# Performance work log

Hardware: AMD Instinct MI355X
Metric: run time of the kernel (lower is better)

Reference implementation:

```python
import jax, jax.numpy as jnp
import numpy as np

B, LQ, E = 4, 8400, 256
HEADS, LEVELS, POINTS = 8, 4, 4
HEAD_DIM = E // HEADS
SHAPES = [(80, 80), (40, 40), (20, 20), (10, 10)]  # (H, W) per level; sum HW = 8400
LV = sum(h * w for h, w in SHAPES)


def setup_inputs() -> dict:
    key = jax.random.key(0)
    ks = jax.random.split(key, 12)
    query = jax.random.normal(ks[0], (B, LQ, E), jnp.float32)
    # per-level normalized reference points in (0.1, 0.9)
    reference_points = 0.1 + 0.8 * jax.random.uniform(ks[1], (B, LQ, LEVELS, 2), jnp.float32)
    value = jax.random.normal(ks[2], (B, LV, E), jnp.float32)
    spatial_shapes = jnp.array(SHAPES, dtype=jnp.int32)
    s = 0.05
    Wv = jax.random.normal(ks[3], (E, E), jnp.float32) * s
    bv = jnp.zeros((E,), jnp.float32)
    Woff = jax.random.normal(ks[4], (E, HEADS * LEVELS * POINTS * 2), jnp.float32) * 0.01
    boff = jax.random.normal(ks[5], (HEADS * LEVELS * POINTS * 2,), jnp.float32) * 0.02
    Wattn = jax.random.normal(ks[6], (E, HEADS * LEVELS * POINTS), jnp.float32) * s
    battn = jnp.zeros((HEADS * LEVELS * POINTS,), jnp.float32)
    Wo = jax.random.normal(ks[7], (E, E), jnp.float32) * s
    bo = jnp.zeros((E,), jnp.float32)
    return dict(query=query, reference_points=reference_points, value=value,
                spatial_shapes=spatial_shapes, Wv=Wv, bv=bv, Woff=Woff, boff=boff,
                Wattn=Wattn, battn=battn, Wo=Wo, bo=bo)


def _bilinear_sample(vflat, x, y, Hl, Wl):
    # vflat: [BH, D, Hl*Wl]; x, y: [BH, N] pixel coords (align_corners=False convention)
    x0f = jnp.floor(x); y0f = jnp.floor(y)
    wx = (x - x0f)[:, None, :]; wy = (y - y0f)[:, None, :]
    x0 = x0f.astype(jnp.int32); y0 = y0f.astype(jnp.int32)

    def gather(ix, iy):
        valid = ((ix >= 0) & (ix < Wl) & (iy >= 0) & (iy < Hl)).astype(vflat.dtype)
        idx = jnp.clip(iy, 0, Hl - 1) * Wl + jnp.clip(ix, 0, Wl - 1)
        g = jnp.take_along_axis(vflat, idx[:, None, :], axis=2)  # [BH, D, N]
        return g * valid[:, None, :]

    v00 = gather(x0, y0); v01 = gather(x0 + 1, y0)
    v10 = gather(x0, y0 + 1); v11 = gather(x0 + 1, y0 + 1)
    return (v00 * (1 - wx) * (1 - wy) + v01 * wx * (1 - wy)
            + v10 * (1 - wx) * wy + v11 * wx * wy)


def _msda_forward(query, reference_points, value, spatial_shapes,
                  Wv, bv, Woff, boff, Wattn, battn, Wo, bo):
    b, lq, _ = query.shape
    v = (value @ Wv + bv).reshape(b, -1, HEADS, HEAD_DIM)
    off = (query @ Woff + boff).reshape(b, lq, HEADS, LEVELS, POINTS, 2)
    aw = (query @ Wattn + battn).reshape(b, lq, HEADS, LEVELS * POINTS)
    aw = jax.nn.softmax(aw, axis=-1).reshape(b, lq, HEADS, LEVELS, POINTS)
    # normalizer (W, H) per level
    norm = jnp.stack([spatial_shapes[:, 1], spatial_shapes[:, 0]], axis=-1).astype(query.dtype)
    # sampling locations in [0,1]: [B, Lq, H, L, P, 2]
    loc = reference_points[:, :, None, :, None, :] + off / norm[None, None, None, :, None, :]

    sampled_levels = []
    start = 0
    for lvl, (Hl, Wl) in enumerate(SHAPES):
        vl = v[:, start:start + Hl * Wl]                      # [B, Hl*Wl, H, D]
        start += Hl * Wl
        vflat = vl.transpose(0, 2, 3, 1).reshape(b * HEADS, HEAD_DIM, Hl * Wl)
        grid = loc[:, :, :, lvl]                              # [B, Lq, H, P, 2]
        grid = grid.transpose(0, 2, 1, 3, 4).reshape(b * HEADS, lq * POINTS, 2)
        g = grid * 2.0 - 1.0                                  # grid_sample convention
        x = (g[..., 0] + 1.0) * (Wl * 0.5) - 0.5
        y = (g[..., 1] + 1.0) * (Hl * 0.5) - 0.5
        s = _bilinear_sample(vflat, x, y, Hl, Wl)             # [BH, D, Lq*P]
        sampled_levels.append(s.reshape(b, HEADS, HEAD_DIM, lq, POINTS))
    sampled = jnp.stack(sampled_levels, axis=-1)              # [B, H, D, Lq, P, L]
    out = jnp.einsum('bhdqpl,bqhlp->bqhd', sampled, aw).reshape(b, lq, E)
    return out @ Wo + bo


def reference(query, reference_points, value, spatial_shapes,
              Wv, bv, Woff, boff, Wattn, battn, Wo, bo):
    return _msda_forward(query, reference_points, value, spatial_shapes,
                         Wv, bv, Woff, boff, Wattn, battn, Wo, bo)
```

## Files before the change

kernel.cpp:

```cpp
#include <hip/hip_runtime.h>
#include <math.h>

#define BB 4
#define LQ 8400
#define NH 8
#define LVTOT 8500
#define HD 32

typedef __attribute__((ext_vector_type(8))) short short8;
typedef __attribute__((ext_vector_type(4))) float f32x4;
typedef __attribute__((ext_vector_type(2))) float f32x2;
typedef __attribute__((ext_vector_type(2))) _Float16 half2_t;
typedef __attribute__((ext_vector_type(2))) __fp16 fp16x2_t;
typedef unsigned short ushort_t;

__device__ __forceinline__ ushort_t f2bf(float f) {
    union { float f; unsigned u; } v; v.f = f;
    unsigned r = v.u + 0x7fffu + ((v.u >> 16) & 1u);
    return (ushort_t)(r >> 16);
}
__device__ __forceinline__ float bflo(unsigned u) {
    union { unsigned u; float f; } x; x.u = u << 16; return x.f;
}
__device__ __forceinline__ float bfhi(unsigned u) {
    union { unsigned u; float f; } x; x.u = u & 0xffff0000u; return x.f;
}
__device__ __forceinline__ half2_t ash2(unsigned u) {
    union { unsigned u; half2_t h; } x; x.u = u; return x.h;
}
__device__ __forceinline__ unsigned pk2u(fp16x2_t h) {
    union { fp16x2_t h; unsigned u; } x; x.h = h; return x.u;
}

__device__ __forceinline__ void dma16(const ushort_t* g, ushort_t* l) {
    __builtin_amdgcn_global_load_lds(
        (const __attribute__((address_space(1))) void*)g,
        (__attribute__((address_space(3))) void*)l, 16, 0, 0);
}

__global__ __launch_bounds__(256) void prep_all(
    const float* __restrict__ value, const float* __restrict__ query,
    const float* __restrict__ Wv, const float* __restrict__ Woff,
    const float* __restrict__ Wattn, const float* __restrict__ Wo,
    ushort_t* __restrict__ value_b, ushort_t* __restrict__ query_b,
    ushort_t* __restrict__ BT)
{
    const int bid = blockIdx.x;
    if (bid < 16900) {
        const float* src = (bid < 8500) ? value : query;
        ushort_t* dst = (bid < 8500) ? value_b : query_b;
        int i = (bid < 8500 ? bid : bid - 8500) * 256 + threadIdx.x;
        float4 f = ((const float4*)src)[i];
        ushort4 o;
        o.x = f2bf(f.x); o.y = f2bf(f.y); o.z = f2bf(f.z); o.w = f2bf(f.w);
        ((ushort4*)dst)[i] = o;
    } else {
        int idx = (bid - 16900) * 256 + threadIdx.x;
        int r = idx >> 8, k = idx & 255;
        float v;
        if (r < 256) v = Wv[k * 256 + r];
        else if (r < 640) {
            int n = r - 256;
            v = (n < 256) ? Woff[k * 256 + n] : Wattn[k * 128 + (n - 256)];
        } else v = Wo[k * 256 + (r - 640)];
        BT[idx] = f2bf(v);
    }
}

__device__ __forceinline__ void gemm_core(
    const ushort_t* __restrict__ A, const ushort_t* __restrict__ B, int M,
    int m0, int n0, ushort_t* Asl, ushort_t* Bsl, f32x4 acc[4][4])
{
    const int tid  = threadIdx.x;
    const int wave = tid >> 6, lane = tid & 63;
    const int quad = lane >> 4, mr = lane & 15;
    const int wm   = (wave >> 1) * 64, wn = (wave & 1) * 64;
    const int oct  = lane >> 3;
    const int bseg = lane & 7;

    for (int k0 = 0; k0 < 256; k0 += 64) {
        __syncthreads();
        #pragma unroll
        for (int i = 0; i < 4; i++) {
            int m  = i * 32 + wave * 8 + oct;
            int gs = bseg ^ (m & 7);
            int am = min(m0 + m, M - 1);
            dma16(A + (size_t)am * 256 + k0 + gs * 8,
                  Asl + (size_t)(i * 32 + wave * 8) * 64 + lane * 8);
            int bn = n0 + m;
            dma16(B + (size_t)bn * 256 + k0 + gs * 8,
                  Bsl + (size_t)(i * 32 + wave * 8) * 64 + lane * 8);
        }
        __syncthreads();
        #pragma unroll
        for (int ks = 0; ks < 2; ks++) {
            short8 af[4], bf[4];
            const int ksl = ks * 4 + quad;
            #pragma unroll
            for (int i = 0; i < 4; i++) {
                int m = wm + i * 16 + mr;
                af[i] = *(const short8*)&Asl[m * 64 + (ksl ^ (m & 7)) * 8];
                int n = wn + i * 16 + mr;
                bf[i] = *(const short8*)&Bsl[n * 64 + (ksl ^ (n & 7)) * 8];
            }
            #pragma unroll
            for (int i = 0; i < 4; i++)
                #pragma unroll
                for (int j = 0; j < 4; j++)
                    acc[i][j] = __builtin_amdgcn_mfma_f32_16x16x32_bf16(
                        af[i], bf[j], acc[i][j], 0, 0, 0);
        }
    }
}

__global__ __launch_bounds__(256, 3) void gemm_fused(
    const ushort_t* __restrict__ Av, const ushort_t* __restrict__ Aq,
    const ushort_t* __restrict__ BT,
    const float* __restrict__ bv, const float* __restrict__ boff,
    const float* __restrict__ battn,
    ushort_t* __restrict__ vperm, ushort_t* __restrict__ off_b,
    ushort_t* __restrict__ awl_b)
{
    __shared__ ushort_t Asl[128 * 64];
    __shared__ ushort_t Bsl[128 * 64];

    const int bid = blockIdx.x;
    int mode, m0, n0, M;
    const ushort_t *A, *B;
    if (bid < 532) { mode = 0; m0 = (bid >> 1) * 128; n0 = (bid & 1) * 128;
                     A = Av; B = BT; M = 34000; }
    else { int b2 = bid - 532;
           mode = 1; m0 = (b2 / 3) * 128; n0 = (b2 % 3) * 128;
           A = Aq; B = BT + 65536; M = 33600; }

    f32x4 acc[4][4];
    #pragma unroll
    for (int i = 0; i < 4; i++)
        #pragma unroll
        for (int j = 0; j < 4; j++) acc[i][j] = (f32x4){0.f, 0.f, 0.f, 0.f};

    gemm_core(A, B, M, m0, n0, Asl, Bsl, acc);

    const int tid  = threadIdx.x;
    const int wave = tid >> 6, lane = tid & 63;
    const int quad = lane >> 4, mr = lane & 15;
    const int wm   = (wave >> 1) * 64, wn = (wave & 1) * 64;

    #pragma unroll
    for (int i = 0; i < 4; i++) {
        const int rbase = m0 + wm + i * 16 + quad * 4;
        #pragma unroll
        for (int j = 0; j < 4; j++) {
            const int c = n0 + wn + j * 16 + mr;
            #pragma unroll
            for (int reg = 0; reg < 4; reg++) {
                int row = rbase + reg;
                if (row >= M) continue;
                float val = acc[i][j][reg];
                if (mode == 0) {
                    float o = val + bv[c];
                    int b = row / LVTOT, pix = row - b * LVTOT;
                    int h = c >> 5, d = c & 31;
                    union { _Float16 h16; ushort_t u; } cv;
                    cv.h16 = (_Float16)o;
                    vperm[(((size_t)(b * NH + h)) * LVTOT + pix) * HD + d] = cv.u;
                } else {
                    if (c < 256) off_b[(size_t)row * 256 + c] = f2bf(val + boff[c]);
                    else awl_b[(size_t)row * 128 + (c - 256)] = f2bf(val + battn[c - 256]);
                }
            }
        }
    }
}

__global__ __launch_bounds__(256, 3) void gemm_out(
    const ushort_t* __restrict__ A, const ushort_t* __restrict__ BT,
    const float* __restrict__ bo, float* __restrict__ out)
{
    __shared__ ushort_t Asl[128 * 64];
    __shared__ ushort_t Bsl[128 * 64];

    const int m0 = (blockIdx.x >> 1) * 128;
    const int n0 = (blockIdx.x & 1) * 128;
    const int M = 33600;

    f32x4 acc[4][4];
    #pragma unroll
    for (int i = 0; i < 4; i++)
        #pragma unroll
        for (int j = 0; j < 4; j++) acc[i][j] = (f32x4){0.f, 0.f, 0.f, 0.f};

    gemm_core(A, BT, M, m0, n0, Asl, Bsl, acc);

    const int tid  = threadIdx.x;
    const int wave = tid >> 6, lane = tid & 63;
    const int quad = lane >> 4, mr = lane & 15;
    const int wm   = (wave >> 1) * 64, wn = (wave & 1) * 64;

    #pragma unroll
    for (int i = 0; i < 4; i++) {
        const int rbase = m0 + wm + i * 16 + quad * 4;
        #pragma unroll
        for (int j = 0; j < 4; j++) {
            const int c = n0 + wn + j * 16 + mr;
            #pragma unroll
            for (int reg = 0; reg < 4; reg++) {
                int row = rbase + reg;
                if (row >= M) continue;
                out[(size_t)row * 256 + c] = acc[i][j][reg] + bo[c];
            }
        }
    }
}

__global__ __launch_bounds__(256) void msda_sample(
    const ushort_t* __restrict__ vperm, const ushort_t* __restrict__ off,
    const ushort_t* __restrict__ awl, const float* __restrict__ refp,
    ushort_t* __restrict__ sampled)
{
    __shared__ uint2 s_w[16 * 33];
    __shared__ int4  s_i[16 * 33];

    const int tid = threadIdx.x;
    const int bid = blockIdx.x;
    const int h   = bid & 7;
    const int r   = bid >> 3;
    const int b   = r / 263;
    const int c   = r - b * 263;
    const int q0b = c * 32;
    const int bq0 = b * LQ + q0b;

    const int Hs[4]   = {80, 40, 20, 10};
    const int base[4] = {0, 6400, 8000, 8400};

    #pragma unroll
    for (int it = 0; it < 2; it++) {
        const int s  = it * 256 + tid;
        const int ql = s >> 4, lp = s & 15;
        const int l  = lp >> 2;
        const int qv = (q0b + ql < LQ) ? ql : 0;
        const size_t bq = (size_t)(bq0 + qv);
        const int Wl = Hs[l];

        unsigned od = *(const unsigned*)(off + bq * 256 + h * 32 + lp * 2);
        float ox = bflo(od), oy = bfhi(od);
        float lgt = bflo((unsigned)awl[bq * 128 + h * 16 + lp]);
        float e = __expf(lgt);
        float sum = e;
        sum += __shfl_xor(sum, 1, 16);
        sum += __shfl_xor(sum, 2, 16);
        sum += __shfl_xor(sum, 4, 16);
        sum += __shfl_xor(sum, 8, 16);
        float aw = e * __builtin_amdgcn_rcpf(sum);

        float2 rp = *(const float2*)(refp + bq * 8 + l * 2);
        float x = rp.x * (float)Wl + ox - 0.5f;
        float y = rp.y * (float)Wl + oy - 0.5f;
        float x0f = floorf(x), y0f = floorf(y);
        float wx = x - x0f, wy = y - y0f;
        int x0 = (int)x0f, y0 = (int)y0f;
        bool vx0 = (x0 >= 0) & (x0 < Wl);
        bool vx1 = (x0 + 1 >= 0) & (x0 + 1 < Wl);
        bool vy0 = (y0 >= 0) & (y0 < Wl);
        bool vy1 = (y0 + 1 >= 0) & (y0 + 1 < Wl);
        int cx0 = min(max(x0, 0), Wl - 1);
        int cx1 = min(max(x0 + 1, 0), Wl - 1);
        int cy0 = min(max(y0, 0), Wl - 1);
        int cy1 = min(max(y0 + 1, 0), Wl - 1);
        float w00 = (vx0 && vy0) ? (1.f - wx) * (1.f - wy) * aw : 0.f;
        float w01 = (vx1 && vy0) ? wx * (1.f - wy) * aw : 0.f;
        float w10 = (vx0 && vy1) ? (1.f - wx) * wy * aw : 0.f;
        float w11 = (vx1 && vy1) ? wx * wy * aw : 0.f;
        const int rec = lp * 33 + ql;
        s_w[rec] = make_uint2(pk2u(__builtin_amdgcn_cvt_pkrtz(w00, w01)),
                              pk2u(__builtin_amdgcn_cvt_pkrtz(w10, w11)));
        s_i[rec] = make_int4((base[l] + cy0 * Wl + cx0) << 6,
                             (base[l] + cy0 * Wl + cx1) << 6,
                             (base[l] + cy1 * Wl + cx0) << 6,
                             (base[l] + cy1 * Wl + cx1) << 6);
    }
    __syncthreads();

    const int ql  = tid >> 3;
    const int l8  = tid & 7;
    const int dby = l8 * 8;

    if (q0b + ql < LQ) {
        const char* plane = (const char*)(vperm + (size_t)(b * NH + h) * (LVTOT * HD));
        float a0 = 0.f, a1 = 0.f, a2 = 0.f, a3 = 0.f;
        #pragma unroll
        for (int pg = 0; pg < 4; pg++) {
            uint2 wv[4]; int4 iv[4];
            #pragma unroll
            for (int t = 0; t < 4; t++) {
                const int rec = (pg * 4 + t) * 33 + ql;
                wv[t] = s_w[rec];
                iv[t] = s_i[rec];
            }
            uint2 g0[4], g1[4], g2[4], g3[4];
            #pragma unroll
            for (int t = 0; t < 4; t++) {
                g0[t] = *(const uint2*)(plane + (unsigned)(iv[t].x + dby));
                g1[t] = *(const uint2*)(plane + (unsigned)(iv[t].y + dby));
                g2[t] = *(const uint2*)(plane + (unsigned)(iv[t].z + dby));
                g3[t] = *(const uint2*)(plane + (unsigned)(iv[t].w + dby));
            }
            #pragma unroll
            for (int t = 0; t < 4; t++) {
                half2_t w01 = ash2(wv[t].x);
                half2_t w23 = ash2(wv[t].y);
                unsigned p01lo = __builtin_amdgcn_perm(g1[t].x, g0[t].x, 0x05040100);
                unsigned p01hi = __builtin_amdgcn_perm(g1[t].x, g0[t].x, 0x07060302);
                unsigned p23lo = __builtin_amdgcn_perm(g3[t].x, g2[t].x, 0x05040100);
                unsigned p23hi = __builtin_amdgcn_perm(g3[t].x, g2[t].x, 0x07060302);
                a0 = __builtin_amdgcn_fdot2(w01, ash2(p01lo), a0, false);
                a0 = __builtin_amdgcn_fdot2(w23, ash2(p23lo), a0, false);
                a1 = __builtin_amdgcn_fdot2(w01, ash2(p01hi), a1, false);
                a1 = __builtin_amdgcn_fdot2(w23, ash2(p23hi), a1, false);
                unsigned q01lo = __builtin_amdgcn_perm(g1[t].y, g0[t].y, 0x05040100);
                unsigned q01hi = __builtin_amdgcn_perm(g1[t].y, g0[t].y, 0x07060302);
                unsigned q23lo = __builtin_amdgcn_perm(g3[t].y, g2[t].y, 0x05040100);
                unsigned q23hi = __builtin_amdgcn_perm(g3[t].y, g2[t].y, 0x07060302);
                a2 = __builtin_amdgcn_fdot2(w01, ash2(q01lo), a2, false);
                a2 = __builtin_amdgcn_fdot2(w23, ash2(q23lo), a2, false);
                a3 = __builtin_amdgcn_fdot2(w01, ash2(q01hi), a3, false);
                a3 = __builtin_amdgcn_fdot2(w23, ash2(q23hi), a3, false);
            }
        }
        const size_t bq = (size_t)(bq0 + ql);
        ushort4 o;
        o.x = f2bf(a0); o.y = f2bf(a1);
        o.z = f2bf(a2); o.w = f2bf(a3);
        *(ushort4*)(sampled + bq * 256 + h * 32 + l8 * 4) = o;
    }
}

extern "C" void kernel_launch(void* const* d_in, const int* in_sizes, int n_in,
                              void* d_out, int out_size, void* d_ws, size_t ws_size,
                              hipStream_t stream) {
    const float* query = (const float*)d_in[0];
    const float* refp  = (const float*)d_in[1];
    const float* value = (const float*)d_in[2];
    const float* Wv    = (const float*)d_in[4];
    const float* bv    = (const float*)d_in[5];
    const float* Woff  = (const float*)d_in[6];
    const float* boff  = (const float*)d_in[7];
    const float* Wattn = (const float*)d_in[8];
    const float* battn = (const float*)d_in[9];
    const float* Wo    = (const float*)d_in[10];
    const float* bo    = (const float*)d_in[11];
    float* out = (float*)d_out;

    ushort_t* ws = (ushort_t*)d_ws;
    ushort_t* off_b   = ws;
    ushort_t* awl_b   = off_b + 8601600;
    ushort_t* value_b = awl_b + 4300800;
    ushort_t* query_b = value_b + 8704000;
    ushort_t* vperm_b = query_b + 8601600;
    ushort_t* BT      = vperm_b + 8704000;
    ushort_t* sampled_b = query_b;

    prep_all<<<dim3(17796), 256, 0, stream>>>(
        value, query, Wv, Woff, Wattn, Wo, value_b, query_b, BT);

    gemm_fused<<<dim3(532 + 789), 256, 0, stream>>>(
        value_b, query_b, BT, bv, boff, battn, vperm_b, off_b, awl_b);

    msda_sample<<<dim3(8 * 4 * 263), 256, 0, stream>>>(
        vperm_b, off_b, awl_b, refp, sampled_b);

    gemm_out<<<dim3(526), 256, 0, stream>>>(
        sampled_b, BT + 163840, bo, out);
}
```

Baseline: 248.1 us.

## Stage coarse value levels in LDS and loop persistent blocks over query chunks

The sampling kernel now launches 512 blocks of 1024 threads. Each block owns one (batch, head) and a 525-query chunk, and first copies levels 1-3 of its value plane (2000 positions x 32 dims, bf16) into LDS via dma16. Level-0 samples still gather from global memory, while levels 1-3 read from LDS. Each query's 16 points are split across two 8-lane halves whose partial sums are combined with a shuffle. Sample-weight and index setup is recomputed per 64-query pass with block barriers, and indices shrink to 16-bit. The aim is to cut global gather traffic and repeated index work, at the cost of ~128KB LDS per block (limiting occupancy), extra barriers, and fewer, larger blocks.

```diff
diff --git a/kernel.cpp b/kernel.cpp
--- a/kernel.cpp
+++ b/kernel.cpp
@@ -6,6 +6,7 @@
 #define NH 8
 #define LVTOT 8500
 #define HD 32
+#define NQB 525
 
 typedef __attribute__((ext_vector_type(8))) short short8;
 typedef __attribute__((ext_vector_type(4))) float f32x4;
@@ -213,33 +214,44 @@
     }
 }
 
-__global__ __launch_bounds__(256) void msda_sample(
+__global__ __launch_bounds__(1024) void msda_sample(
     const ushort_t* __restrict__ vperm, const ushort_t* __restrict__ off,
     const ushort_t* __restrict__ awl, const float* __restrict__ refp,
     ushort_t* __restrict__ sampled)
 {
-    __shared__ uint2 s_w[16 * 33];
-    __shared__ int4  s_i[16 * 33];
-
-    const int tid = threadIdx.x;
-    const int bid = blockIdx.x;
-    const int h   = bid & 7;
-    const int r   = bid >> 3;
-    const int b   = r / 263;
-    const int c   = r - b * 263;
-    const int q0b = c * 32;
-    const int bq0 = b * LQ + q0b;
-
-    const int Hs[4]   = {80, 40, 20, 10};
-    const int base[4] = {0, 6400, 8000, 8400};
-
-    #pragma unroll
-    for (int it = 0; it < 2; it++) {
-        const int s  = it * 256 + tid;
-        const int ql = s >> 4, lp = s & 15;
+    __shared__ ushort_t lds_v[2000 * HD];
+    __shared__ uint2    s_w[64 * 17];
+    __shared__ ushort4  s_iv[64 * 17];
+
+    const int tid   = threadIdx.x;
+    const int bid   = blockIdx.x;
+    const int h     = bid & 7;
+    const int b     = (bid >> 3) & 3;
+    const int chunk = bid >> 5;
+    const int q0    = chunk * NQB;
+    const size_t bq0 = (size_t)b * LQ + q0;
+
+    const ushort_t* plane = vperm + (size_t)(b * NH + h) * (LVTOT * HD);
+
+    {
+        const ushort_t* psrc = plane + 6400 * HD;
+        #pragma unroll
+        for (int it = 0; it < 8; it++) {
+            int i = it * 1024 + tid;
+            if (i < 8000) dma16(psrc + i * 8, lds_v + i * 8);
+        }
+    }
+
+    const int Hs[4]    = {80, 40, 20, 10};
+    const int base2[4] = {0, 0, 1600, 8400};
+
+    const int NPASS = (NQB + 63) / 64;
+
+    {
+        const int ql = tid >> 4, lp = tid & 15;
         const int l  = lp >> 2;
-        const int qv = (q0b + ql < LQ) ? ql : 0;
-        const size_t bq = (size_t)(bq0 + qv);
+        const int lq = min(ql, NQB - 1);
+        const size_t bq = bq0 + lq;
         const int Wl = Hs[l];
 
         unsigned od = *(const unsigned*)(off + bq * 256 + h * 32 + lp * 2);
@@ -271,67 +283,150 @@
         float w01 = (vx1 && vy0) ? wx * (1.f - wy) * aw : 0.f;
         float w10 = (vx0 && vy1) ? (1.f - wx) * wy * aw : 0.f;
         float w11 = (vx1 && vy1) ? wx * wy * aw : 0.f;
-        const int rec = lp * 33 + ql;
+        const int rec = ql * 17 + lp;
+        const int bs = base2[l];
         s_w[rec] = make_uint2(pk2u(__builtin_amdgcn_cvt_pkrtz(w00, w01)),
                               pk2u(__builtin_amdgcn_cvt_pkrtz(w10, w11)));
-        s_i[rec] = make_int4((base[l] + cy0 * Wl + cx0) << 6,
-                             (base[l] + cy0 * Wl + cx1) << 6,
-                             (base[l] + cy1 * Wl + cx0) << 6,
-                             (base[l] + cy1 * Wl + cx1) << 6);
+        s_iv[rec] = make_ushort4((ushort_t)(bs + cy0 * Wl + cx0),
+                                 (ushort_t)(bs + cy0 * Wl + cx1),
+                                 (ushort_t)(bs + cy1 * Wl + cx0),
+                                 (ushort_t)(bs + cy1 * Wl + cx1));
     }
     __syncthreads();
 
-    const int ql  = tid >> 3;
-    const int l8  = tid & 7;
-    const int dby = l8 * 8;
-
-    if (q0b + ql < LQ) {
-        const char* plane = (const char*)(vperm + (size_t)(b * NH + h) * (LVTOT * HD));
-        float a0 = 0.f, a1 = 0.f, a2 = 0.f, a3 = 0.f;
-        #pragma unroll
-        for (int pg = 0; pg < 4; pg++) {
-            uint2 wv[4]; int4 iv[4];
-            #pragma unroll
-            for (int t = 0; t < 4; t++) {
-                const int rec = (pg * 4 + t) * 33 + ql;
-                wv[t] = s_w[rec];
-                iv[t] = s_i[rec];
-            }
-            uint2 g0[4], g1[4], g2[4], g3[4];
-            #pragma unroll
-            for (int t = 0; t < 4; t++) {
-                g0[t] = *(const uint2*)(plane + (unsigned)(iv[t].x + dby));
-                g1[t] = *(const uint2*)(plane + (unsigned)(iv[t].y + dby));
-                g2[t] = *(const uint2*)(plane + (unsigned)(iv[t].z + dby));
-                g3[t] = *(const uint2*)(plane + (unsigned)(iv[t].w + dby));
-            }
-            #pragma unroll
-            for (int t = 0; t < 4; t++) {
-                half2_t w01 = ash2(wv[t].x);
-                half2_t w23 = ash2(wv[t].y);
-                unsigned p01lo = __builtin_amdgcn_perm(g1[t].x, g0[t].x, 0x05040100);
-                unsigned p01hi = __builtin_amdgcn_perm(g1[t].x, g0[t].x, 0x07060302);
-                unsigned p23lo = __builtin_amdgcn_perm(g3[t].x, g2[t].x, 0x05040100);
-                unsigned p23hi = __builtin_amdgcn_perm(g3[t].x, g2[t].x, 0x07060302);
+    for (int p = 0; ; p++) {
+        {
+            const int ql  = tid >> 4;
+            const int sub = tid & 15;
+            const int g   = sub >> 3;
+            const int dsh = (sub & 7) * 4;
+            const int dby = (sub & 7) * 8;
+            const int lq  = p * 64 + ql;
+
+            float a0 = 0.f, a1 = 0.f, a2 = 0.f, a3 = 0.f;
+
+            uint2 gw[4]; ushort4 giv[4];
+            uint2 gv0[4], gv1[4], gv2[4], gv3[4];
+            #pragma unroll
+            for (int pi = 0; pi < 4; pi++) {
+                const int pt = g ? (12 + pi) : pi;
+                const int rec = ql * 17 + pt;
+                gw[pi]  = s_w[rec];
+                giv[pi] = s_iv[rec];
+                gv0[pi] = *(const uint2*)((const char*)plane + (((unsigned)giv[pi].x << 6) + dby));
+                gv1[pi] = *(const uint2*)((const char*)plane + (((unsigned)giv[pi].y << 6) + dby));
+                gv2[pi] = *(const uint2*)((const char*)plane + (((unsigned)giv[pi].z << 6) + dby));
+                gv3[pi] = *(const uint2*)((const char*)plane + (((unsigned)giv[pi].w << 6) + dby));
+            }
+            #pragma unroll
+            for (int pi = 0; pi < 4; pi++) {
+                const int pt = g ? (8 + pi) : (4 + pi);
+                const int rec = ql * 17 + pt;
+                uint2 w = s_w[rec];
+                ushort4 iv = s_iv[rec];
+                uint2 v0 = *(const uint2*)&lds_v[(unsigned)iv.x * HD + dsh];
+                uint2 v1 = *(const uint2*)&lds_v[(unsigned)iv.y * HD + dsh];
+                uint2 v2 = *(const uint2*)&lds_v[(unsigned)iv.z * HD + dsh];
+                uint2 v3 = *(const uint2*)&lds_v[(unsigned)iv.w * HD + dsh];
+                half2_t w01 = ash2(w.x), w23 = ash2(w.y);
+                unsigned p01lo = __builtin_amdgcn_perm(v1.x, v0.x, 0x05040100);
+                unsigned p01hi = __builtin_amdgcn_perm(v1.x, v0.x, 0x07060302);
+                unsigned p23lo = __builtin_amdgcn_perm(v3.x, v2.x, 0x05040100);
+                unsigned p23hi = __builtin_amdgcn_perm(v3.x, v2.x, 0x07060302);
                 a0 = __builtin_amdgcn_fdot2(w01, ash2(p01lo), a0, false);
                 a0 = __builtin_amdgcn_fdot2(w23, ash2(p23lo), a0, false);
                 a1 = __builtin_amdgcn_fdot2(w01, ash2(p01hi), a1, false);
                 a1 = __builtin_amdgcn_fdot2(w23, ash2(p23hi), a1, false);
-                unsigned q01lo = __builtin_amdgcn_perm(g1[t].y, g0[t].y, 0x05040100);
-                unsigned q01hi = __builtin_amdgcn_perm(g1[t].y, g0[t].y, 0x07060302);
-                unsigned q23lo = __builtin_amdgcn_perm(g3[t].y, g2[t].y, 0x05040100);
-                unsigned q23hi = __builtin_amdgcn_perm(g3[t].y, g2[t].y, 0x07060302);
+                unsigned q01lo = __builtin_amdgcn_perm(v1.y, v0.y, 0x05040100);
+                unsigned q01hi = __builtin_amdgcn_perm(v1.y, v0.y, 0x07060302);
+                unsigned q23lo = __builtin_amdgcn_perm(v3.y, v2.y, 0x05040100);
+                unsigned q23hi = __builtin_amdgcn_perm(v3.y, v2.y, 0x07060302);
                 a2 = __builtin_amdgcn_fdot2(w01, ash2(q01lo), a2, false);
                 a2 = __builtin_amdgcn_fdot2(w23, ash2(q23lo), a2, false);
                 a3 = __builtin_amdgcn_fdot2(w01, ash2(q01hi), a3, false);
                 a3 = __builtin_amdgcn_fdot2(w23, ash2(q23hi), a3, false);
             }
-        }
-        const size_t bq = (size_t)(bq0 + ql);
-        ushort4 o;
-        o.x = f2bf(a0); o.y = f2bf(a1);
-        o.z = f2bf(a2); o.w = f2bf(a3);
-        *(ushort4*)(sampled + bq * 256 + h * 32 + l8 * 4) = o;
+            #pragma unroll
+            for (int pi = 0; pi < 4; pi++) {
+                half2_t w01 = ash2(gw[pi].x), w23 = ash2(gw[pi].y);
+                unsigned p01lo = __builtin_amdgcn_perm(gv1[pi].x, gv0[pi].x, 0x05040100);
+                unsigned p01hi = __builtin_amdgcn_perm(gv1[pi].x, gv0[pi].x, 0x07060302);
+                unsigned p23lo = __builtin_amdgcn_perm(gv3[pi].x, gv2[pi].x, 0x05040100);
+                unsigned p23hi = __builtin_amdgcn_perm(gv3[pi].x, gv2[pi].x, 0x07060302);
+                a0 = __builtin_amdgcn_fdot2(w01, ash2(p01lo), a0, false);
+                a0 = __builtin_amdgcn_fdot2(w23, ash2(p23lo), a0, false);
+                a1 = __builtin_amdgcn_fdot2(w01, ash2(p01hi), a1, false);
+                a1 = __builtin_amdgcn_fdot2(w23, ash2(p23hi), a1, false);
+                unsigned q01lo = __builtin_amdgcn_perm(gv1[pi].y, gv0[pi].y, 0x05040100);
+                unsigned q01hi = __builtin_amdgcn_perm(gv1[pi].y, gv0[pi].y, 0x07060302);
+                unsigned q23lo = __builtin_amdgcn_perm(gv3[pi].y, gv2[pi].y, 0x05040100);
+                unsigned q23hi = __builtin_amdgcn_perm(gv3[pi].y, gv2[pi].y, 0x07060302);
+                a2 = __builtin_amdgcn_fdot2(w01, ash2(q01lo), a2, false);
+                a2 = __builtin_amdgcn_fdot2(w23, ash2(q23lo), a2, false);
+                a3 = __builtin_amdgcn_fdot2(w01, ash2(q01hi), a3, false);
+                a3 = __builtin_amdgcn_fdot2(w23, ash2(q23hi), a3, false);
+            }
+            a0 += __shfl_xor(a0, 8);
+            a1 += __shfl_xor(a1, 8);
+            a2 += __shfl_xor(a2, 8);
+            a3 += __shfl_xor(a3, 8);
+            if (sub < 8 && lq < NQB) {
+                const size_t bq = bq0 + lq;
+                ushort4 o;
+                o.x = f2bf(a0); o.y = f2bf(a1);
+                o.z = f2bf(a2); o.w = f2bf(a3);
+                *(ushort4*)(sampled + bq * 256 + h * 32 + dsh) = o;
+            }
+        }
+        if (p + 1 >= NPASS) break;
+        __syncthreads();
+
+        {
+            const int ql = tid >> 4, lp = tid & 15;
+            const int l  = lp >> 2;
+            const int lq = min((p + 1) * 64 + ql, NQB - 1);
+            const size_t bq = bq0 + lq;
+            const int Wl = Hs[l];
+
+            unsigned od = *(const unsigned*)(off + bq * 256 + h * 32 + lp * 2);
+            float ox = bflo(od), oy = bfhi(od);
+            float lgt = bflo((unsigned)awl[bq * 128 + h * 16 + lp]);
+            float e = __expf(lgt);
+            float sum = e;
+            sum += __shfl_xor(sum, 1, 16);
+            sum += __shfl_xor(sum, 2, 16);
+            sum += __shfl_xor(sum, 4, 16);
+            sum += __shfl_xor(sum, 8, 16);
+            float aw = e * __builtin_amdgcn_rcpf(sum);
+
+            float2 rp = *(const float2*)(refp + bq * 8 + l * 2);
+            float x = rp.x * (float)Wl + ox - 0.5f;
+            float y = rp.y * (float)Wl + oy - 0.5f;
+            float x0f = floorf(x), y0f = floorf(y);
+            float wx = x - x0f, wy = y - y0f;
+            int x0 = (int)x0f, y0 = (int)y0f;
+            bool vx0 = (x0 >= 0) & (x0 < Wl);
+            bool vx1 = (x0 + 1 >= 0) & (x0 + 1 < Wl);
+            bool vy0 = (y0 >= 0) & (y0 < Wl);
+            bool vy1 = (y0 + 1 >= 0) & (y0 + 1 < Wl);
+            int cx0 = min(max(x0, 0), Wl - 1);
+            int cx1 = min(max(x0 + 1, 0), Wl - 1);
+            int cy0 = min(max(y0, 0), Wl - 1);
+            int cy1 = min(max(y0 + 1, 0), Wl - 1);
+            float w00 = (vx0 && vy0) ? (1.f - wx) * (1.f - wy) * aw : 0.f;
+            float w01 = (vx1 && vy0) ? wx * (1.f - wy) * aw : 0.f;
+            float w10 = (vx0 && vy1) ? (1.f - wx) * wy * aw : 0.f;
+            float w11 = (vx1 && vy1) ? wx * wy * aw : 0.f;
+            const int rec = ql * 17 + lp;
+            const int bs = base2[l];
+            s_w[rec] = make_uint2(pk2u(__builtin_amdgcn_cvt_pkrtz(w00, w01)),
+                                  pk2u(__builtin_amdgcn_cvt_pkrtz(w10, w11)));
+            s_iv[rec] = make_ushort4((ushort_t)(bs + cy0 * Wl + cx0),
+                                     (ushort_t)(bs + cy0 * Wl + cx1),
+                                     (ushort_t)(bs + cy1 * Wl + cx0),
+                                     (ushort_t)(bs + cy1 * Wl + cx1));
+        }
+        __syncthreads();
     }
 }
 
@@ -366,7 +461,7 @@
     gemm_fused<<<dim3(532 + 789), 256, 0, stream>>>(
         value_b, query_b, BT, bv, boff, battn, vperm_b, off_b, awl_b);
 
-    msda_sample<<<dim3(8 * 4 * 263), 256, 0, stream>>>(
+    msda_sample<<<dim3(512), 1024, 0, stream>>>(
         vperm_b, off_b, awl_b, refp, sampled_b);
 
     gemm_out<<<dim3(526), 256, 0, stream>>>(
```

Result: no change. 248.1 us (-0.0%).

## Store value as duplicated interleaved horizontal pixel pairs for 2-load bilinear gathers

Applied to the files above, without the earlier changes.

The value projection epilogue now writes each pixel twice into a pair-interleaved layout: pixels (x, x+1) are packed per channel in two copies, one for even and one for odd pair starts. The sampler can then fetch both horizontal neighbours with one 16-byte load per row, so each bilinear sample needs two gathers instead of four and no byte permutes. Weights and offsets are combined into one shared-memory record. In exchange the value buffer doubles in size and the GEMM epilogue does twice the scattered writes plus extra index arithmetic.

```diff
diff --git a/kernel.cpp b/kernel.cpp
--- a/kernel.cpp
+++ b/kernel.cpp
@@ -6,10 +6,10 @@
 #define NH 8
 #define LVTOT 8500
 #define HD 32
+#define PLANE_USH 544000
 
 typedef __attribute__((ext_vector_type(8))) short short8;
 typedef __attribute__((ext_vector_type(4))) float f32x4;
-typedef __attribute__((ext_vector_type(2))) float f32x2;
 typedef __attribute__((ext_vector_type(2))) _Float16 half2_t;
 typedef __attribute__((ext_vector_type(2))) __fp16 fp16x2_t;
 typedef unsigned short ushort_t;
@@ -163,7 +163,19 @@
                     int h = c >> 5, d = c & 31;
                     union { _Float16 h16; ushort_t u; } cv;
                     cv.h16 = (_Float16)o;
-                    vperm[(((size_t)(b * NH + h)) * LVTOT + pix) * HD + d] = cv.u;
+                    int lb, y, x, rowp;
+                    if (pix < 6400)      { int rel = pix;        y = rel / 80; x = rel - y * 80; rowp = 40; lb = 0; }
+                    else if (pix < 8000) { int rel = pix - 6400; y = rel / 40; x = rel - y * 40; rowp = 20; lb = 3200; }
+                    else if (pix < 8400) { int rel = pix - 8000; y = rel / 20; x = rel - y * 20; rowp = 10; lb = 4000; }
+                    else                 { int rel = pix - 8400; y = rel / 10; x = rel - y * 10; rowp = 5;  lb = 4200; }
+                    size_t plane = (size_t)(b * NH + h) * PLANE_USH;
+                    int yb = lb + y * rowp;
+                    int i0 = (yb + (x >> 1)) * 64 + d * 2 + (x & 1);
+                    int p1 = x ? ((x - 1) >> 1) : (rowp - 1);
+                    int s1 = x ? ((x - 1) & 1) : 1;
+                    int i1 = (4250 + yb + p1) * 64 + d * 2 + s1;
+                    vperm[plane + i0] = cv.u;
+                    vperm[plane + i1] = cv.u;
                 } else {
                     if (c < 256) off_b[(size_t)row * 256 + c] = f2bf(val + boff[c]);
                     else awl_b[(size_t)row * 128 + (c - 256)] = f2bf(val + battn[c - 256]);
@@ -218,8 +230,7 @@
     const ushort_t* __restrict__ awl, const float* __restrict__ refp,
     ushort_t* __restrict__ sampled)
 {
-    __shared__ uint2 s_w[16 * 33];
-    __shared__ int4  s_i[16 * 33];
+    __shared__ int4 s_wi[16 * 33];
 
     const int tid = threadIdx.x;
     const int bid = blockIdx.x;
@@ -228,10 +239,10 @@
     const int b   = r / 263;
     const int c   = r - b * 263;
     const int q0b = c * 32;
-    const int bq0 = b * LQ + q0b;
-
-    const int Hs[4]   = {80, 40, 20, 10};
-    const int base[4] = {0, 6400, 8000, 8400};
+    const size_t bq0 = (size_t)b * LQ + q0b;
+
+    const int Hs[4]    = {80, 40, 20, 10};
+    const int pbase[4] = {0, 3200, 4000, 4200};
 
     #pragma unroll
     for (int it = 0; it < 2; it++) {
@@ -239,7 +250,7 @@
         const int ql = s >> 4, lp = s & 15;
         const int l  = lp >> 2;
         const int qv = (q0b + ql < LQ) ? ql : 0;
-        const size_t bq = (size_t)(bq0 + qv);
+        const size_t bq = bq0 + qv;
         const int Wl = Hs[l];
 
         unsigned od = *(const unsigned*)(off + bq * 256 + h * 32 + lp * 2);
@@ -259,75 +270,53 @@
         float x0f = floorf(x), y0f = floorf(y);
         float wx = x - x0f, wy = y - y0f;
         int x0 = (int)x0f, y0 = (int)y0f;
-        bool vx0 = (x0 >= 0) & (x0 < Wl);
-        bool vx1 = (x0 + 1 >= 0) & (x0 + 1 < Wl);
-        bool vy0 = (y0 >= 0) & (y0 < Wl);
-        bool vy1 = (y0 + 1 >= 0) & (y0 + 1 < Wl);
-        int cx0 = min(max(x0, 0), Wl - 1);
-        int cx1 = min(max(x0 + 1, 0), Wl - 1);
+        float hx0 = ((x0 >= 0) & (x0 < Wl)) ? (1.f - wx) : 0.f;
+        float hx1 = ((x0 + 1 >= 0) & (x0 + 1 < Wl)) ? wx : 0.f;
+        float vy0w = ((y0 >= 0) & (y0 < Wl)) ? (1.f - wy) * aw : 0.f;
+        float vy1w = ((y0 + 1 >= 0) & (y0 + 1 < Wl)) ? wy * aw : 0.f;
+        int px = min(max(x0, 0), Wl - 2);
+        float pl, pr;
+        if (x0 < px)      { pl = hx1; pr = 0.f; }
+        else if (x0 > px) { pl = 0.f; pr = hx0; }
+        else              { pl = hx0; pr = hx1; }
         int cy0 = min(max(y0, 0), Wl - 1);
         int cy1 = min(max(y0 + 1, 0), Wl - 1);
-        float w00 = (vx0 && vy0) ? (1.f - wx) * (1.f - wy) * aw : 0.f;
-        float w01 = (vx1 && vy0) ? wx * (1.f - wy) * aw : 0.f;
-        float w10 = (vx0 && vy1) ? (1.f - wx) * wy * aw : 0.f;
-        float w11 = (vx1 && vy1) ? wx * wy * aw : 0.f;
-        const int rec = lp * 33 + ql;
-        s_w[rec] = make_uint2(pk2u(__builtin_amdgcn_cvt_pkrtz(w00, w01)),
-                              pk2u(__builtin_amdgcn_cvt_pkrtz(w10, w11)));
-        s_i[rec] = make_int4((base[l] + cy0 * Wl + cx0) << 6,
-                             (base[l] + cy0 * Wl + cx1) << 6,
-                             (base[l] + cy1 * Wl + cx0) << 6,
-                             (base[l] + cy1 * Wl + cx1) << 6);
+        const int copy = px & 1;
+        const int p    = copy ? ((px - 1) >> 1) : (px >> 1);
+        const int rowp = Wl >> 1;
+        const int cb   = copy * 4250 + pbase[l] + p;
+        const int otop = (cb + cy0 * rowp) << 7;
+        const int obot = (cb + cy1 * rowp) << 7;
+        unsigned wt = pk2u(__builtin_amdgcn_cvt_pkrtz(pl * vy0w, pr * vy0w));
+        unsigned wb = pk2u(__builtin_amdgcn_cvt_pkrtz(pl * vy1w, pr * vy1w));
+        s_wi[lp * 33 + ql] = make_int4((int)wt, (int)wb, otop, obot);
     }
     __syncthreads();
 
     const int ql  = tid >> 3;
     const int l8  = tid & 7;
-    const int dby = l8 * 8;
+    const int dby = l8 * 16;
 
     if (q0b + ql < LQ) {
-        const char* plane = (const char*)(vperm + (size_t)(b * NH + h) * (LVTOT * HD));
+        const char* plane = (const char*)(vperm + (size_t)(b * NH + h) * PLANE_USH);
         float a0 = 0.f, a1 = 0.f, a2 = 0.f, a3 = 0.f;
         #pragma unroll
-        for (int pg = 0; pg < 4; pg++) {
-            uint2 wv[4]; int4 iv[4];
-            #pragma unroll
-            for (int t = 0; t < 4; t++) {
-                const int rec = (pg * 4 + t) * 33 + ql;
-                wv[t] = s_w[rec];
-                iv[t] = s_i[rec];
-            }
-            uint2 g0[4], g1[4], g2[4], g3[4];
-            #pragma unroll
-            for (int t = 0; t < 4; t++) {
-                g0[t] = *(const uint2*)(plane + (unsigned)(iv[t].x + dby));
-                g1[t] = *(const uint2*)(plane + (unsigned)(iv[t].y + dby));
-                g2[t] = *(const uint2*)(plane + (unsigned)(iv[t].z + dby));
-                g3[t] = *(const uint2*)(plane + (unsigned)(iv[t].w + dby));
-            }
-            #pragma unroll
-            for (int t = 0; t < 4; t++) {
-                half2_t w01 = ash2(wv[t].x);
-                half2_t w23 = ash2(wv[t].y);
-                unsigned p01lo = __builtin_amdgcn_perm(g1[t].x, g0[t].x, 0x05040100);
-                unsigned p01hi = __builtin_amdgcn_perm(g1[t].x, g0[t].x, 0x07060302);
-                unsigned p23lo = __builtin_amdgcn_perm(g3[t].x, g2[t].x, 0x05040100);
-                unsigned p23hi = __builtin_amdgcn_perm(g3[t].x, g2[t].x, 0x07060302);
-                a0 = __builtin_amdgcn_fdot2(w01, ash2(p01lo), a0, false);
-                a0 = __builtin_amdgcn_fdot2(w23, ash2(p23lo), a0, false);
-                a1 = __builtin_amdgcn_fdot2(w01, ash2(p01hi), a1, false);
-                a1 = __builtin_amdgcn_fdot2(w23, ash2(p23hi), a1, false);
-                unsigned q01lo = __builtin_amdgcn_perm(g1[t].y, g0[t].y, 0x05040100);
-                unsigned q01hi = __builtin_amdgcn_perm(g1[t].y, g0[t].y, 0x07060302);
-                unsigned q23lo = __builtin_amdgcn_perm(g3[t].y, g2[t].y, 0x05040100);
-                unsigned q23hi = __builtin_amdgcn_perm(g3[t].y, g2[t].y, 0x07060302);
-                a2 = __builtin_amdgcn_fdot2(w01, ash2(q01lo), a2, false);
-                a2 = __builtin_amdgcn_fdot2(w23, ash2(q23lo), a2, false);
-                a3 = __builtin_amdgcn_fdot2(w01, ash2(q01hi), a3, false);
-                a3 = __builtin_amdgcn_fdot2(w23, ash2(q23hi), a3, false);
-            }
-        }
-        const size_t bq = (size_t)(bq0 + ql);
+        for (int pt = 0; pt < 16; pt++) {
+            int4 wi = s_wi[pt * 33 + ql];
+            uint4 vt = *(const uint4*)(plane + (unsigned)(wi.z + dby));
+            uint4 vb = *(const uint4*)(plane + (unsigned)(wi.w + dby));
+            half2_t wt = ash2((unsigned)wi.x);
+            half2_t wb = ash2((unsigned)wi.y);
+            a0 = __builtin_amdgcn_fdot2(wt, ash2(vt.x), a0, false);
+            a0 = __builtin_amdgcn_fdot2(wb, ash2(vb.x), a0, false);
+            a1 = __builtin_amdgcn_fdot2(wt, ash2(vt.y), a1, false);
+            a1 = __builtin_amdgcn_fdot2(wb, ash2(vb.y), a1, false);
+            a2 = __builtin_amdgcn_fdot2(wt, ash2(vt.z), a2, false);
+            a2 = __builtin_amdgcn_fdot2(wb, ash2(vb.z), a2, false);
+            a3 = __builtin_amdgcn_fdot2(wt, ash2(vt.w), a3, false);
+            a3 = __builtin_amdgcn_fdot2(wb, ash2(vb.w), a3, false);
+        }
+        const size_t bq = bq0 + ql;
         ushort4 o;
         o.x = f2bf(a0); o.y = f2bf(a1);
         o.z = f2bf(a2); o.w = f2bf(a3);
@@ -357,7 +346,7 @@
     ushort_t* value_b = awl_b + 4300800;
     ushort_t* query_b = value_b + 8704000;
     ushort_t* vperm_b = query_b + 8601600;
-    ushort_t* BT      = vperm_b + 8704000;
+    ushort_t* BT      = vperm_b + 17408000;
     ushort_t* sampled_b = query_b;
 
     prep_all<<<dim3(17796), 256, 0, stream>>>(
```

Result: faster. 228.0 us (-8.1%).
